# Kernel tuning notes

Measured on AMD Instinct MI355X. Metric: run time of the kernel, lower is better.

The kernel has to match this reference:

```python
import jax, jax.numpy as jnp
import numpy as np

SL, BS, D, H = 2048, 4, 512, 8
NH = D // H  # per-head dim (nhid)
SCALE = np.float32(1.0 / np.sqrt(NH))


def setup_inputs() -> dict:
    key = jax.random.key(0)
    ks = jax.random.split(key, 8)
    s = np.float32(0.02)
    return {
        "input_tensor": jax.random.normal(ks[0], (SL, BS, D), jnp.float32),
        "keys_vector": jax.random.normal(ks[1], (SL, BS, D), jnp.float32),
        "values_vector": jax.random.normal(ks[2], (SL, BS, D), jnp.float32),
        # learned projections: query/keys/values -> num_heads*nhid, plus output proj
        "Wq": jax.random.normal(ks[3], (D, D), jnp.float32) * s,
        "bq": jnp.zeros((D,), jnp.float32),
        "Wk": jax.random.normal(ks[4], (D, D), jnp.float32) * s,
        "bk": jnp.zeros((D,), jnp.float32),
        "Wv": jax.random.normal(ks[5], (D, D), jnp.float32) * s,
        "bv": jnp.zeros((D,), jnp.float32),
        "Wo": jax.random.normal(ks[6], (D, D), jnp.float32) * s,
        "bo": jnp.zeros((D,), jnp.float32),
    }


def reference(input_tensor, keys_vector, values_vector, Wq, bq, Wk, bk, Wv, bv, Wo, bo):
    # Vectorized equivalent of the per-step Python loop with incremental mask
    # (mask=True): query step i attends to keys 0..i -> causal attention.
    q = (input_tensor @ Wq + bq).reshape(SL, BS, H, NH)   # [q,b,h,n]
    k = (keys_vector @ Wk + bk).reshape(SL, BS, H, NH)    # [s,b,h,n]
    v = (values_vector @ Wv + bv).reshape(SL, BS, H, NH)  # [s,b,h,n]
    scores = jnp.einsum('qbhn,sbhn->qsbh', q, k) * SCALE  # [q,s,b,h]
    causal = jnp.tril(jnp.ones((SL, SL), dtype=bool))     # allow s <= q
    scores = jnp.where(causal[:, :, None, None], scores, jnp.float32(-1e9))
    w = jax.nn.softmax(scores, axis=1)                    # softmax over keys s
    out = jnp.einsum('qsbh,sbhn->qbhn', w, v).reshape(SL, BS, D)
    return out @ Wo + bo                                  # [q,b,D]
```

## Files before the change

### kernel.cpp

```cpp
#include <hip/hip_runtime.h>

typedef __attribute__((ext_vector_type(8))) short short8;
typedef __attribute__((ext_vector_type(4))) short short4v;
typedef __attribute__((ext_vector_type(4))) float f32x4;
typedef __attribute__((ext_vector_type(2))) unsigned int uint2v;

constexpr int SL = 2048, BS = 4, D = 512, H = 8, NH = 64;
constexpr int M_ROWS = SL * BS;
constexpr float SCALE = 0.125f;
constexpr float LOG2E = 1.44269504088896340736f;

__device__ __forceinline__ unsigned short f2bf(float f) {
  union { float f; unsigned u; } v; v.f = f;
  unsigned r = v.u + 0x7FFFu + ((v.u >> 16) & 1u);
  return (unsigned short)(r >> 16);
}

__device__ __forceinline__ unsigned cvt_pk_bf16(float a, float b) {
  unsigned r;
  asm("v_cvt_pk_bf16_f32 %0, %1, %2" : "=v"(r) : "v"(a), "v"(b));
  return r;
}

__device__ __forceinline__ float fast_exp2(float x) {
  float r;
  asm("v_exp_f32 %0, %1" : "=v"(r) : "v"(x));
  return r;
}

__device__ __forceinline__ void gl16(const void* g, void* l) {
  __builtin_amdgcn_global_load_lds(
      (const __attribute__((address_space(1))) unsigned int*)g,
      (__attribute__((address_space(3))) unsigned int*)l, 16, 0, 0);
}

__global__ __launch_bounds__(256) void prep_wt(
    const float* __restrict__ w0, const float* __restrict__ w1,
    const float* __restrict__ w2, const float* __restrict__ w3,
    unsigned short* __restrict__ wtb) {
  __shared__ float tl[64][65];
  const int tid = threadIdx.x;
  const int wi = blockIdx.x >> 6, t6 = blockIdx.x & 63;
  const int k0 = (t6 >> 3) * 64, n0 = (t6 & 7) * 64;
  const float* W = wi == 0 ? w0 : (wi == 1 ? w1 : (wi == 2 ? w2 : w3));
  unsigned short* WT = wtb + (size_t)wi * D * D;

#pragma unroll
  for (int i = 0; i < 4; ++i) {
    int k = (tid >> 4) + i * 16, n4 = (tid & 15) * 4;
    f32x4 v = *reinterpret_cast<const f32x4*>(&W[(size_t)(k0 + k) * D + n0 + n4]);
#pragma unroll
    for (int j = 0; j < 4; ++j) tl[n4 + j][k] = v[j];
  }
  __syncthreads();
#pragma unroll
  for (int i = 0; i < 2; ++i) {
    int n = (tid >> 3) + i * 32, k8 = (tid & 7) * 8;
    union { unsigned u[4]; short8 s; } pk;
#pragma unroll
    for (int j = 0; j < 4; ++j)
      pk.u[j] = cvt_pk_bf16(tl[n][k8 + 2 * j], tl[n][k8 + 2 * j + 1]);
    *reinterpret_cast<short8*>(&WT[(size_t)(n0 + n) * D + k0 + k8]) = pk.s;
  }
}

template <bool A_BF16, int OUT_MODE>
__device__ __forceinline__ void gemm_bt_body(const void* __restrict__ Ap,
                                             const unsigned short* __restrict__ BT,
                                             const float* __restrict__ bias,
                                             void* __restrict__ Outp, float scale,
                                             unsigned short* smem) {
  const int tid = threadIdx.x;
  const int brow = blockIdx.x * 128;
  const int bcol = blockIdx.y * 64;
  const int lane = tid & 63;
  const int wid = tid >> 6;
  const int wr = (wid >> 1) * 64;
  const int wc = (wid & 1) * 32;
  const int r = lane & 15;
  const int g = lane >> 4;

  auto a_buf = [&](int b) { return smem + b * 8192; };
  auto b_buf = [&](int b) { return smem + 16384 + b * 4096; };

  f32x4 acc[4][2];
#pragma unroll
  for (int m = 0; m < 4; ++m)
#pragma unroll
    for (int n = 0; n < 2; ++n) acc[m][n] = f32x4{0.f, 0.f, 0.f, 0.f};

  auto STAGE_B = [&](int kt, int bsel) {
    unsigned short* bl = b_buf(bsel);
#pragma unroll
    for (int j = 0; j < 2; ++j) {
      int c = j * 256 + tid;
      int row = c >> 3, c8 = (c & 7) ^ (row & 7);
      gl16(&BT[(size_t)(bcol + row) * D + kt + c8 * 8], &bl[c * 8]);
    }
  };
  auto STAGE_A_LDS = [&](int kt, int bsel) {
    const unsigned short* A = (const unsigned short*)Ap;
    unsigned short* al = a_buf(bsel);
#pragma unroll
    for (int j = 0; j < 4; ++j) {
      int c = j * 256 + tid;
      int row = c >> 3, c8 = (c & 7) ^ (row & 7);
      gl16(&A[(size_t)(brow + row) * D + kt + c8 * 8], &al[c * 8]);
    }
  };
  auto A_LOAD = [&](int kt, f32x4 (&va)[4][2]) {
    const float* A = (const float*)Ap;
#pragma unroll
    for (int j = 0; j < 4; ++j) {
      int c = j * 256 + tid;
      int row = c >> 3, c8 = (c & 7) ^ (row & 7);
      const float* ap = &A[(size_t)(brow + row) * D + kt + c8 * 8];
      va[j][0] = *reinterpret_cast<const f32x4*>(ap);
      va[j][1] = *reinterpret_cast<const f32x4*>(ap + 4);
    }
  };
  auto A_WRITE = [&](f32x4 (&va)[4][2], int bsel) {
    unsigned short* al = a_buf(bsel);
#pragma unroll
    for (int j = 0; j < 4; ++j) {
      int c = j * 256 + tid;
      union { unsigned u[4]; short8 s; } pk;
      pk.u[0] = cvt_pk_bf16(va[j][0][0], va[j][0][1]);
      pk.u[1] = cvt_pk_bf16(va[j][0][2], va[j][0][3]);
      pk.u[2] = cvt_pk_bf16(va[j][1][0], va[j][1][1]);
      pk.u[3] = cvt_pk_bf16(va[j][1][2], va[j][1][3]);
      *reinterpret_cast<short8*>(&al[c * 8]) = pk.s;
    }
  };
  auto COMPUTE = [&](int bsel) {
    const unsigned short* al = a_buf(bsel);
    const unsigned short* bl = b_buf(bsel);
#pragma unroll
    for (int kk2 = 0; kk2 < 2; ++kk2) {
      short8 af[4], bfr[2];
#pragma unroll
      for (int m = 0; m < 4; ++m)
        af[m] = *reinterpret_cast<const short8*>(
            &al[(wr + m * 16 + r) * 64 + (((kk2 * 4 + g) ^ (r & 7)) * 8)]);
#pragma unroll
      for (int n = 0; n < 2; ++n)
        bfr[n] = *reinterpret_cast<const short8*>(
            &bl[(wc + n * 16 + r) * 64 + (((kk2 * 4 + g) ^ (r & 7)) * 8)]);
      __builtin_amdgcn_s_setprio(1);
#pragma unroll
      for (int m = 0; m < 4; ++m)
#pragma unroll
        for (int n = 0; n < 2; ++n)
          acc[m][n] = __builtin_amdgcn_mfma_f32_16x16x32_bf16(af[m], bfr[n], acc[m][n], 0, 0, 0);
      __builtin_amdgcn_s_setprio(0);
    }
  };

  if (A_BF16) {
    STAGE_A_LDS(0, 0);
    STAGE_B(0, 0);
    asm volatile("s_waitcnt vmcnt(0)" ::: "memory");
  } else {
    f32x4 va[4][2];
    A_LOAD(0, va);
    STAGE_B(0, 0);
    asm volatile("s_waitcnt vmcnt(2)" ::: "memory");
    A_WRITE(va, 0);
    asm volatile("s_waitcnt vmcnt(0) lgkmcnt(0)" ::: "memory");
  }
  __builtin_amdgcn_s_barrier();

#pragma unroll
  for (int t = 0; t < 8; ++t) {
    const int cur = t & 1, nxt = cur ^ 1;
    const int ktn = (t + 1) * 64;
    __builtin_amdgcn_sched_barrier(0);
    f32x4 va[4][2];
    if (t < 7) {
      if (A_BF16) {
        STAGE_A_LDS(ktn, nxt);
        STAGE_B(ktn, nxt);
      } else {
        A_LOAD(ktn, va);
        STAGE_B(ktn, nxt);
      }
    }
    __builtin_amdgcn_sched_barrier(0);
    COMPUTE(cur);
    if (t < 7) {
      if (!A_BF16) {
        asm volatile("s_waitcnt vmcnt(2)" ::: "memory");
        A_WRITE(va, nxt);
      }
      asm volatile("s_waitcnt vmcnt(0) lgkmcnt(0)" ::: "memory");
      __builtin_amdgcn_s_barrier();
    }
  }

  if (OUT_MODE == 2) {
    __syncthreads();
    unsigned short* sc = smem;
    const int wr4 = wr >> 2;
#pragma unroll
    for (int m = 0; m < 4; ++m)
#pragma unroll
      for (int n = 0; n < 2; ++n) {
        int col = wc + n * 16 + r;
        float bv = bias[bcol + col];
        int sl = wr4 + m * 4 + g;
        int pp = ((sl >> 2) & 3) * 8 + ((sl >> 4) & 1) * 4 + (sl & 3);
#pragma unroll
        for (int rr = 0; rr < 4; ++rr) {
          int c = (rr * 4 + (pp >> 3)) ^ (col & 7);
          sc[col * 128 + c * 8 + (pp & 7)] = f2bf((acc[m][n][rr] + bv) * scale);
        }
      }
    asm volatile("s_waitcnt lgkmcnt(0)" ::: "memory");
    __builtin_amdgcn_s_barrier();
    unsigned short* VT = (unsigned short*)Outp;
    {
      int q = tid;
      int col = q >> 2, bb = q & 3;
      int gcol = bcol + col, hh = gcol >> 6, nh = gcol & 63;
      size_t gbase = (((size_t)bb * H + hh) * NH + nh) * SL + (brow >> 2);
#pragma unroll
      for (int j = 0; j < 4; ++j) {
        short8 v = *reinterpret_cast<const short8*>(
            &sc[col * 128 + (((bb * 4 + j) ^ (col & 7)) * 8)]);
        *reinterpret_cast<short8*>(&VT[gbase + j * 8]) = v;
      }
    }
  } else {
#pragma unroll
    for (int m = 0; m < 4; ++m)
#pragma unroll
      for (int n = 0; n < 2; ++n) {
        int gcol = bcol + wc + n * 16 + r;
        float bv = bias[gcol];
#pragma unroll
        for (int rr = 0; rr < 4; ++rr) {
          int grow = brow + wr + m * 16 + g * 4 + rr;
          float val = (acc[m][n][rr] + bv) * scale;
          if (OUT_MODE == 0)
            ((float*)Outp)[(size_t)grow * D + gcol] = val;
          else
            ((unsigned short*)Outp)[(size_t)grow * D + gcol] = f2bf(val);
        }
      }
  }
}

__global__ __launch_bounds__(256) void qkv_gemm(
    const float* __restrict__ x0, const float* __restrict__ x1, const float* __restrict__ x2,
    const unsigned short* __restrict__ wtb,
    const float* __restrict__ b0, const float* __restrict__ b1, const float* __restrict__ b2,
    unsigned short* __restrict__ q_out, unsigned short* __restrict__ k_out,
    unsigned short* __restrict__ vt_out) {
  __shared__ __align__(16) unsigned short smem[24576];
  int z = blockIdx.z;
  const float* X = z == 0 ? x0 : (z == 1 ? x1 : x2);
  const unsigned short* WT = wtb + (size_t)z * D * D;
  const float* B = z == 0 ? b0 : (z == 1 ? b1 : b2);
  float scale = (z == 0) ? SCALE * LOG2E : 1.0f;
  if (z == 2)
    gemm_bt_body<false, 2>(X, WT, B, vt_out, scale, smem);
  else
    gemm_bt_body<false, 1>(X, WT, B, z == 0 ? q_out : k_out, scale, smem);
}

__global__ __launch_bounds__(256) void gemm_oproj(
    const unsigned short* __restrict__ A, const unsigned short* __restrict__ WT,
    const float* __restrict__ B, float* __restrict__ Outp) {
  __shared__ __align__(16) unsigned short smem[24576];
  gemm_bt_body<true, 0>(A, WT, B, Outp, 1.0f, smem);
}

__global__ __launch_bounds__(256, 3) void flash_attn(
    const unsigned short* __restrict__ Q, const unsigned short* __restrict__ K,
    const unsigned short* __restrict__ Vt, unsigned short* __restrict__ O) {
  __shared__ __align__(16) unsigned short k_lds[3][64 * 64];
  __shared__ __align__(16) unsigned short v_lds[3][64 * 64];

  const int bid = blockIdx.x;
  const int s = bid >> 5, idx = bid & 31;
  const int grp = idx & 7;
  const int bh = grp * 4 + (idx >> 3);
  const int b = bh >> 3, h = bh & 7;
  const int qt = (s < 8) ? 31 - s : (s < 16) ? s + 8 : (s < 24) ? 31 - s : s - 24;
  const int q0 = qt * 64;

  const int tid = threadIdx.x;
  const int w = tid >> 6, lane = tid & 63;
  const int r = lane & 15, g = lane >> 4;
  const int swz = (r & 7) << 3;

  const unsigned short* Qb = Q + (size_t)b * D + h * NH;
  const unsigned short* Kb = K + (size_t)b * D + h * NH;
  const unsigned short* Vb = Vt + ((size_t)(b * H + h) * NH) * SL;
  unsigned short* Ob = O + (size_t)b * D + h * NH;

  auto STAGE = [&](int kt, int bsel) {
    unsigned short* kl = &k_lds[bsel][0];
    unsigned short* vl = &v_lds[bsel][0];
#pragma unroll
    for (int j = 0; j < 2; ++j) {
      int c = j * 256 + tid;
      int row = c >> 3, c8 = (c & 7) ^ (row & 7);
      gl16(&Kb[(size_t)(kt * 64 + row) * (BS * D) + c8 * 8], &kl[c * 8]);
      gl16(&Vb[(size_t)row * SL + kt * 64 + c8 * 8], &vl[c * 8]);
    }
  };

  STAGE(0, 0);
  if (qt >= 1) STAGE(1, 1);

  short8 qf[2];
#pragma unroll
  for (int kk = 0; kk < 2; ++kk)
    qf[kk] = *reinterpret_cast<const short8*>(
        &Qb[(size_t)(q0 + w * 16 + r) * (BS * D) + kk * 32 + g * 8]);

  f32x4 oa[4];
#pragma unroll
  for (int n = 0; n < 4; ++n) oa[n] = f32x4{0.f, 0.f, 0.f, 0.f};
  float mr = -1e30f, lrp = 0.f;

  int bsel = 0;
  for (int kt = 0; kt <= qt; ++kt) {
    if (kt < qt)
      asm volatile("s_waitcnt vmcnt(8)" ::: "memory");
    else
      asm volatile("s_waitcnt vmcnt(0)" ::: "memory");
    __builtin_amdgcn_s_barrier();
    __builtin_amdgcn_sched_barrier(0);
    if (kt + 2 <= qt) {
      int nb = bsel + 2; if (nb >= 3) nb -= 3;
      STAGE(kt + 2, nb);
    }

    const unsigned short* kl = &k_lds[bsel][0];
    const unsigned short* vl = &v_lds[bsel][0];
    short8 kf[2][4];
#pragma unroll
    for (int kk = 0; kk < 2; ++kk)
#pragma unroll
      for (int n = 0; n < 4; ++n)
        kf[kk][n] = *reinterpret_cast<const short8*>(
            &kl[(n * 16 + r) * 64 + ((kk * 32 + g * 8) ^ swz)]);

    f32x4 sv[4];
#pragma unroll
    for (int n = 0; n < 4; ++n) sv[n] = f32x4{0.f, 0.f, 0.f, 0.f};
#pragma unroll
    for (int kk = 0; kk < 2; ++kk)
#pragma unroll
      for (int n = 0; n < 4; ++n)
        sv[n] = __builtin_amdgcn_mfma_f32_16x16x32_bf16(kf[kk][n], qf[kk], sv[n], 0, 0, 0);

    short8 vt[2][4];
#pragma unroll
    for (int kk = 0; kk < 2; ++kk)
#pragma unroll
      for (int n = 0; n < 4; ++n)
        vt[kk][n] = *reinterpret_cast<const short8*>(
            &vl[(n * 16 + r) * 64 + ((kk * 32 + g * 8) ^ swz)]);

    if (kt == qt) {
      int qrow = q0 + w * 16 + r;
#pragma unroll
      for (int n = 0; n < 4; ++n)
#pragma unroll
        for (int rr = 0; rr < 4; ++rr)
          if (kt * 64 + n * 16 + g * 4 + rr > qrow) sv[n][rr] = -1e30f;
    }

    float t0 = fmaxf(fmaxf(sv[0][0], sv[0][1]), sv[0][2]);
    float t1 = fmaxf(fmaxf(sv[0][3], sv[1][0]), sv[1][1]);
    float t2 = fmaxf(fmaxf(sv[1][2], sv[1][3]), sv[2][0]);
    float t3 = fmaxf(fmaxf(sv[2][1], sv[2][2]), sv[2][3]);
    float t4 = fmaxf(fmaxf(sv[3][0], sv[3][1]), sv[3][2]);
    float mxl = fmaxf(fmaxf(fmaxf(t0, t1), fmaxf(t2, t3)), fmaxf(t4, sv[3][3]));
    bool need = __any(mxl > mr + 8.f);
    float mold = mr;
    float mnew = mold;
    if (need) {
      float mx = fmaxf(mxl, __shfl_xor(mxl, 16));
      mx = fmaxf(mx, __shfl_xor(mx, 32));
      mnew = fmaxf(mold, mx);
    }
#pragma unroll
    for (int n = 0; n < 4; ++n)
#pragma unroll
      for (int rr = 0; rr < 4; ++rr)
        sv[n][rr] = fast_exp2(sv[n][rr] - mnew);
    float a0 = (sv[0][0] + sv[0][1]) + (sv[0][2] + sv[0][3]);
    float a1 = (sv[1][0] + sv[1][1]) + (sv[1][2] + sv[1][3]);
    float a2 = (sv[2][0] + sv[2][1]) + (sv[2][2] + sv[2][3]);
    float a3 = (sv[3][0] + sv[3][1]) + (sv[3][2] + sv[3][3]);
    float psl = (a0 + a1) + (a2 + a3);
    if (need) {
      float sf = fast_exp2(mold - mnew);
      mr = mnew;
      lrp = lrp * sf + psl;
#pragma unroll
      for (int n = 0; n < 4; ++n) oa[n] *= sf;
    } else {
      lrp += psl;
    }

    short8 pf[2];
#pragma unroll
    for (int kk = 0; kk < 2; ++kk) {
      union { unsigned u[4]; short8 s8; } P;
      P.u[0] = cvt_pk_bf16(sv[2 * kk][0], sv[2 * kk][1]);
      P.u[1] = cvt_pk_bf16(sv[2 * kk][2], sv[2 * kk][3]);
      P.u[2] = cvt_pk_bf16(sv[2 * kk + 1][0], sv[2 * kk + 1][1]);
      P.u[3] = cvt_pk_bf16(sv[2 * kk + 1][2], sv[2 * kk + 1][3]);
      pf[kk] = P.s8;
    }

#pragma unroll
    for (int kk = 0; kk < 2; ++kk)
#pragma unroll
      for (int n = 0; n < 4; ++n)
        oa[n] = __builtin_amdgcn_mfma_f32_16x16x32_bf16(vt[kk][n], pf[kk], oa[n], 0, 0, 0);

    ++bsel; if (bsel >= 3) bsel = 0;
  }

  __syncthreads();
  {
    unsigned short* pw = &k_lds[0][0] + w * 2048;
    float lr = lrp + __shfl_xor(lrp, 16);
    lr += __shfl_xor(lr, 32);
    float inv = 1.0f / lr;
#pragma unroll
    for (int n = 0; n < 4; ++n) {
      uint2v pk;
      pk.x = cvt_pk_bf16(oa[n][0] * inv, oa[n][1] * inv);
      pk.y = cvt_pk_bf16(oa[n][2] * inv, oa[n][3] * inv);
      *reinterpret_cast<uint2v*>(&pw[r * 64 + ((n * 16 + g * 4) ^ swz)]) = pk;
    }
    asm volatile("s_waitcnt lgkmcnt(0)" ::: "memory");
    __builtin_amdgcn_sched_barrier(0);
#pragma unroll
    for (int i2 = 0; i2 < 2; ++i2) {
      int c = i2 * 64 + lane;
      int row = c >> 3, c8 = c & 7;
      short8 v = *reinterpret_cast<const short8*>(&pw[row * 64 + c8 * 8]);
      *reinterpret_cast<short8*>(
          &Ob[(size_t)(q0 + w * 16 + row) * (BS * D) + ((c8 ^ (row & 7)) * 8)]) = v;
    }
  }
}

extern "C" void kernel_launch(void* const* d_in, const int* in_sizes, int n_in,
                              void* d_out, int out_size, void* d_ws, size_t ws_size,
                              hipStream_t stream) {
  const float* x  = (const float*)d_in[0];
  const float* kx = (const float*)d_in[1];
  const float* vx = (const float*)d_in[2];
  const float* Wq = (const float*)d_in[3];
  const float* bq = (const float*)d_in[4];
  const float* Wk = (const float*)d_in[5];
  const float* bk = (const float*)d_in[6];
  const float* Wv = (const float*)d_in[7];
  const float* bv = (const float*)d_in[8];
  const float* Wo = (const float*)d_in[9];
  const float* bo = (const float*)d_in[10];

  unsigned short* ws = (unsigned short*)d_ws;
  unsigned short* qb  = ws;
  unsigned short* kb  = ws + (size_t)M_ROWS * D;
  unsigned short* vtb = ws + (size_t)M_ROWS * D * 2;
  unsigned short* wtb = ws + (size_t)M_ROWS * D * 3;

  prep_wt<<<dim3(256), dim3(256), 0, stream>>>(Wq, Wk, Wv, Wo, wtb);
  qkv_gemm<<<dim3(64, 8, 3), dim3(256), 0, stream>>>(x, kx, vx, wtb, bq, bk, bv,
                                                     qb, kb, vtb);
  flash_attn<<<dim3(1024), dim3(256), 0, stream>>>(qb, kb, vtb, qb);
  gemm_oproj<<<dim3(64, 8, 1), dim3(256), 0, stream>>>(qb, wtb + (size_t)3 * D * D,
                                                       bo, (float*)d_out);
}
```

Measured before the change: 80.30 us.

## Deepen GEMM k-loop pipeline to prefetch two tiles ahead with triple buffering

Restructures the shared GEMM body so global-to-LDS staging runs two k-tiles ahead instead of one. The oproj path uses three A and three B LDS buffers, and the QKV path keeps register-staged A double-buffered while B is triple-buffered. Partial vmcnt waits replace the full drains before each barrier, aiming to hide global load latency behind MFMA compute. This raises LDS usage per block, which may reduce occupancy, and relies on hand-tuned waitcnt values being correct.

After: 83.27 us. 1.04x slower.

```diff
diff --git a/kernel.cpp b/kernel.cpp
--- a/kernel.cpp
+++ b/kernel.cpp
@@ -80,8 +80,9 @@
   const int r = lane & 15;
   const int g = lane >> 4;
 
+  constexpr int A_BUFS = A_BF16 ? 3 : 2;
   auto a_buf = [&](int b) { return smem + b * 8192; };
-  auto b_buf = [&](int b) { return smem + 16384 + b * 4096; };
+  auto b_buf = [&](int b) { return smem + A_BUFS * 8192 + b * 4096; };
 
   f32x4 acc[4][2];
 #pragma unroll
@@ -132,8 +133,8 @@
       *reinterpret_cast<short8*>(&al[c * 8]) = pk.s;
     }
   };
-  auto COMPUTE = [&](int bsel) {
-    const unsigned short* al = a_buf(bsel);
+  auto COMPUTE = [&](int asel, int bsel) {
+    const unsigned short* al = a_buf(asel);
     const unsigned short* bl = b_buf(bsel);
 #pragma unroll
     for (int kk2 = 0; kk2 < 2; ++kk2) {
@@ -157,43 +158,49 @@
   };
 
   if (A_BF16) {
-    STAGE_A_LDS(0, 0);
-    STAGE_B(0, 0);
-    asm volatile("s_waitcnt vmcnt(0)" ::: "memory");
+    STAGE_A_LDS(0, 0);  STAGE_B(0, 0);
+    STAGE_A_LDS(64, 1); STAGE_B(64, 1);
+    asm volatile("s_waitcnt vmcnt(6)" ::: "memory");
+    __builtin_amdgcn_s_barrier();
+#pragma unroll
+    for (int t = 0; t < 8; ++t) {
+      __builtin_amdgcn_sched_barrier(0);
+      if (t < 6) { STAGE_A_LDS((t + 2) * 64, (t + 2) % 3); STAGE_B((t + 2) * 64, (t + 2) % 3); }
+      __builtin_amdgcn_sched_barrier(0);
+      COMPUTE(t % 3, t % 3);
+      if (t < 7) {
+        if (t < 6) asm volatile("s_waitcnt vmcnt(6)" ::: "memory");
+        else       asm volatile("s_waitcnt vmcnt(0)" ::: "memory");
+        __builtin_amdgcn_s_barrier();
+      }
+    }
   } else {
     f32x4 va[4][2];
     A_LOAD(0, va);
     STAGE_B(0, 0);
-    asm volatile("s_waitcnt vmcnt(2)" ::: "memory");
+    STAGE_B(64, 1);
+    asm volatile("s_waitcnt vmcnt(4)" ::: "memory");
     A_WRITE(va, 0);
-    asm volatile("s_waitcnt vmcnt(0) lgkmcnt(0)" ::: "memory");
-  }
-  __builtin_amdgcn_s_barrier();
-
-#pragma unroll
-  for (int t = 0; t < 8; ++t) {
-    const int cur = t & 1, nxt = cur ^ 1;
-    const int ktn = (t + 1) * 64;
-    __builtin_amdgcn_sched_barrier(0);
-    f32x4 va[4][2];
-    if (t < 7) {
-      if (A_BF16) {
-        STAGE_A_LDS(ktn, nxt);
-        STAGE_B(ktn, nxt);
-      } else {
-        A_LOAD(ktn, va);
-        STAGE_B(ktn, nxt);
-      }
-    }
-    __builtin_amdgcn_sched_barrier(0);
-    COMPUTE(cur);
-    if (t < 7) {
-      if (!A_BF16) {
-        asm volatile("s_waitcnt vmcnt(2)" ::: "memory");
-        A_WRITE(va, nxt);
-      }
-      asm volatile("s_waitcnt vmcnt(0) lgkmcnt(0)" ::: "memory");
-      __builtin_amdgcn_s_barrier();
+    A_LOAD(64, va);
+    asm volatile("s_waitcnt vmcnt(10)" ::: "memory");
+    asm volatile("s_waitcnt lgkmcnt(0)" ::: "memory");
+    __builtin_amdgcn_s_barrier();
+#pragma unroll
+    for (int t = 0; t < 8; ++t) {
+      __builtin_amdgcn_sched_barrier(0);
+      if (t < 6) STAGE_B((t + 2) * 64, (t + 2) % 3);
+      if (t < 7) {
+        if (t < 6) asm volatile("s_waitcnt vmcnt(2)" ::: "memory");
+        else       asm volatile("s_waitcnt vmcnt(0)" ::: "memory");
+        A_WRITE(va, (t + 1) & 1);
+        if (t < 6) A_LOAD((t + 2) * 64, va);
+      }
+      __builtin_amdgcn_sched_barrier(0);
+      COMPUTE(t & 1, t % 3);
+      if (t < 7) {
+        asm volatile("s_waitcnt lgkmcnt(0)" ::: "memory");
+        __builtin_amdgcn_s_barrier();
+      }
     }
   }
 
@@ -256,7 +263,7 @@
     const float* __restrict__ b0, const float* __restrict__ b1, const float* __restrict__ b2,
     unsigned short* __restrict__ q_out, unsigned short* __restrict__ k_out,
     unsigned short* __restrict__ vt_out) {
-  __shared__ __align__(16) unsigned short smem[24576];
+  __shared__ __align__(16) unsigned short smem[2 * 8192 + 3 * 4096];
   int z = blockIdx.z;
   const float* X = z == 0 ? x0 : (z == 1 ? x1 : x2);
   const unsigned short* WT = wtb + (size_t)z * D * D;
@@ -271,7 +278,7 @@
 __global__ __launch_bounds__(256) void gemm_oproj(
     const unsigned short* __restrict__ A, const unsigned short* __restrict__ WT,
     const float* __restrict__ B, float* __restrict__ Outp) {
-  __shared__ __align__(16) unsigned short smem[24576];
+  __shared__ __align__(16) unsigned short smem[3 * 8192 + 3 * 4096];
   gemm_bt_body<true, 0>(A, WT, B, Outp, 1.0f, smem);
 }
 
```

## Pre-convert activations to bf16 and use triple-buffered async-LDS GEMM

Applied to the files above, without the earlier changes.

Adds a standalone kernel that converts the three fp32 activation inputs to bf16 into scratch buffers (reusing d_out and the q/k workspaces with carefully ordered launches). The fused QKV GEMM is split into three bf16 GEMM launches that stage A via global_load_lds instead of register loads plus conversion. The GEMM pipeline moves from double to triple buffering with partial vmcnt waits so two k-tiles stay in flight. This costs an extra pass over the activations in memory and more kernel launches, and reduces grid parallelism per launch compared with the single z=3 launch.

Measured after the change: 91.95 us. 14.5% more time.

```diff
diff --git a/kernel.cpp b/kernel.cpp
--- a/kernel.cpp
+++ b/kernel.cpp
@@ -32,6 +32,27 @@
   __builtin_amdgcn_global_load_lds(
       (const __attribute__((address_space(1))) unsigned int*)g,
       (__attribute__((address_space(3))) unsigned int*)l, 16, 0, 0);
+}
+
+__global__ __launch_bounds__(256) void conv3(
+    const float* __restrict__ x0, const float* __restrict__ x1,
+    const float* __restrict__ x2,
+    unsigned short* __restrict__ d0, unsigned short* __restrict__ d1,
+    unsigned short* __restrict__ d2) {
+  const int u = blockIdx.x * 256 + threadIdx.x;
+#pragma unroll
+  for (int z = 0; z < 3; ++z) {
+    const float* src = z == 0 ? x0 : (z == 1 ? x1 : x2);
+    unsigned short* dst = z == 0 ? d0 : (z == 1 ? d1 : d2);
+    f32x4 v0 = *reinterpret_cast<const f32x4*>(&src[(size_t)u * 8]);
+    f32x4 v1 = *reinterpret_cast<const f32x4*>(&src[(size_t)u * 8 + 4]);
+    union { unsigned uu[4]; short8 s; } pk;
+    pk.uu[0] = cvt_pk_bf16(v0[0], v0[1]);
+    pk.uu[1] = cvt_pk_bf16(v0[2], v0[3]);
+    pk.uu[2] = cvt_pk_bf16(v1[0], v1[1]);
+    pk.uu[3] = cvt_pk_bf16(v1[2], v1[3]);
+    *reinterpret_cast<short8*>(&dst[(size_t)u * 8]) = pk.s;
+  }
 }
 
 __global__ __launch_bounds__(256) void prep_wt(
@@ -64,12 +85,12 @@
   }
 }
 
-template <bool A_BF16, int OUT_MODE>
-__device__ __forceinline__ void gemm_bt_body(const void* __restrict__ Ap,
-                                             const unsigned short* __restrict__ BT,
-                                             const float* __restrict__ bias,
-                                             void* __restrict__ Outp, float scale,
-                                             unsigned short* smem) {
+template <int OUT_MODE>
+__global__ __launch_bounds__(256) void gemm_bf16(
+    const unsigned short* __restrict__ Abf,
+    const unsigned short* __restrict__ BT,
+    const float* __restrict__ bias, void* __restrict__ Outp, float scale) {
+  __shared__ __align__(16) unsigned short smem[3 * 8192 + 3 * 4096];
   const int tid = threadIdx.x;
   const int brow = blockIdx.x * 128;
   const int bcol = blockIdx.y * 64;
@@ -81,7 +102,7 @@
   const int g = lane >> 4;
 
   auto a_buf = [&](int b) { return smem + b * 8192; };
-  auto b_buf = [&](int b) { return smem + 16384 + b * 4096; };
+  auto b_buf = [&](int b) { return smem + 3 * 8192 + b * 4096; };
 
   f32x4 acc[4][2];
 #pragma unroll
@@ -89,6 +110,15 @@
 #pragma unroll
     for (int n = 0; n < 2; ++n) acc[m][n] = f32x4{0.f, 0.f, 0.f, 0.f};
 
+  auto STAGE_A = [&](int kt, int bsel) {
+    unsigned short* al = a_buf(bsel);
+#pragma unroll
+    for (int j = 0; j < 4; ++j) {
+      int c = j * 256 + tid;
+      int row = c >> 3, c8 = (c & 7) ^ (row & 7);
+      gl16(&Abf[(size_t)(brow + row) * D + kt + c8 * 8], &al[c * 8]);
+    }
+  };
   auto STAGE_B = [&](int kt, int bsel) {
     unsigned short* bl = b_buf(bsel);
 #pragma unroll
@@ -98,40 +128,6 @@
       gl16(&BT[(size_t)(bcol + row) * D + kt + c8 * 8], &bl[c * 8]);
     }
   };
-  auto STAGE_A_LDS = [&](int kt, int bsel) {
-    const unsigned short* A = (const unsigned short*)Ap;
-    unsigned short* al = a_buf(bsel);
-#pragma unroll
-    for (int j = 0; j < 4; ++j) {
-      int c = j * 256 + tid;
-      int row = c >> 3, c8 = (c & 7) ^ (row & 7);
-      gl16(&A[(size_t)(brow + row) * D + kt + c8 * 8], &al[c * 8]);
-    }
-  };
-  auto A_LOAD = [&](int kt, f32x4 (&va)[4][2]) {
-    const float* A = (const float*)Ap;
-#pragma unroll
-    for (int j = 0; j < 4; ++j) {
-      int c = j * 256 + tid;
-      int row = c >> 3, c8 = (c & 7) ^ (row & 7);
-      const float* ap = &A[(size_t)(brow + row) * D + kt + c8 * 8];
-      va[j][0] = *reinterpret_cast<const f32x4*>(ap);
-      va[j][1] = *reinterpret_cast<const f32x4*>(ap + 4);
-    }
-  };
-  auto A_WRITE = [&](f32x4 (&va)[4][2], int bsel) {
-    unsigned short* al = a_buf(bsel);
-#pragma unroll
-    for (int j = 0; j < 4; ++j) {
-      int c = j * 256 + tid;
-      union { unsigned u[4]; short8 s; } pk;
-      pk.u[0] = cvt_pk_bf16(va[j][0][0], va[j][0][1]);
-      pk.u[1] = cvt_pk_bf16(va[j][0][2], va[j][0][3]);
-      pk.u[2] = cvt_pk_bf16(va[j][1][0], va[j][1][1]);
-      pk.u[3] = cvt_pk_bf16(va[j][1][2], va[j][1][3]);
-      *reinterpret_cast<short8*>(&al[c * 8]) = pk.s;
-    }
-  };
   auto COMPUTE = [&](int bsel) {
     const unsigned short* al = a_buf(bsel);
     const unsigned short* bl = b_buf(bsel);
@@ -156,43 +152,19 @@
     }
   };
 
-  if (A_BF16) {
-    STAGE_A_LDS(0, 0);
-    STAGE_B(0, 0);
-    asm volatile("s_waitcnt vmcnt(0)" ::: "memory");
-  } else {
-    f32x4 va[4][2];
-    A_LOAD(0, va);
-    STAGE_B(0, 0);
-    asm volatile("s_waitcnt vmcnt(2)" ::: "memory");
-    A_WRITE(va, 0);
-    asm volatile("s_waitcnt vmcnt(0) lgkmcnt(0)" ::: "memory");
-  }
+  STAGE_A(0, 0);  STAGE_B(0, 0);
+  STAGE_A(64, 1); STAGE_B(64, 1);
+  asm volatile("s_waitcnt vmcnt(6)" ::: "memory");
   __builtin_amdgcn_s_barrier();
-
 #pragma unroll
   for (int t = 0; t < 8; ++t) {
-    const int cur = t & 1, nxt = cur ^ 1;
-    const int ktn = (t + 1) * 64;
     __builtin_amdgcn_sched_barrier(0);
-    f32x4 va[4][2];
+    if (t < 6) { STAGE_A((t + 2) * 64, (t + 2) % 3); STAGE_B((t + 2) * 64, (t + 2) % 3); }
+    __builtin_amdgcn_sched_barrier(0);
+    COMPUTE(t % 3);
     if (t < 7) {
-      if (A_BF16) {
-        STAGE_A_LDS(ktn, nxt);
-        STAGE_B(ktn, nxt);
-      } else {
-        A_LOAD(ktn, va);
-        STAGE_B(ktn, nxt);
-      }
-    }
-    __builtin_amdgcn_sched_barrier(0);
-    COMPUTE(cur);
-    if (t < 7) {
-      if (!A_BF16) {
-        asm volatile("s_waitcnt vmcnt(2)" ::: "memory");
-        A_WRITE(va, nxt);
-      }
-      asm volatile("s_waitcnt vmcnt(0) lgkmcnt(0)" ::: "memory");
+      if (t < 6) asm volatile("s_waitcnt vmcnt(6)" ::: "memory");
+      else       asm volatile("s_waitcnt vmcnt(0)" ::: "memory");
       __builtin_amdgcn_s_barrier();
     }
   }
@@ -248,31 +220,6 @@
         }
       }
   }
-}
-
-__global__ __launch_bounds__(256) void qkv_gemm(
-    const float* __restrict__ x0, const float* __restrict__ x1, const float* __restrict__ x2,
-    const unsigned short* __restrict__ wtb,
-    const float* __restrict__ b0, const float* __restrict__ b1, const float* __restrict__ b2,
-    unsigned short* __restrict__ q_out, unsigned short* __restrict__ k_out,
-    unsigned short* __restrict__ vt_out) {
-  __shared__ __align__(16) unsigned short smem[24576];
-  int z = blockIdx.z;
-  const float* X = z == 0 ? x0 : (z == 1 ? x1 : x2);
-  const unsigned short* WT = wtb + (size_t)z * D * D;
-  const float* B = z == 0 ? b0 : (z == 1 ? b1 : b2);
-  float scale = (z == 0) ? SCALE * LOG2E : 1.0f;
-  if (z == 2)
-    gemm_bt_body<false, 2>(X, WT, B, vt_out, scale, smem);
-  else
-    gemm_bt_body<false, 1>(X, WT, B, z == 0 ? q_out : k_out, scale, smem);
-}
-
-__global__ __launch_bounds__(256) void gemm_oproj(
-    const unsigned short* __restrict__ A, const unsigned short* __restrict__ WT,
-    const float* __restrict__ B, float* __restrict__ Outp) {
-  __shared__ __align__(16) unsigned short smem[24576];
-  gemm_bt_body<true, 0>(A, WT, B, Outp, 1.0f, smem);
 }
 
 __global__ __launch_bounds__(256, 3) void flash_attn(
@@ -474,11 +421,13 @@
   unsigned short* kb  = ws + (size_t)M_ROWS * D;
   unsigned short* vtb = ws + (size_t)M_ROWS * D * 2;
   unsigned short* wtb = ws + (size_t)M_ROWS * D * 3;
+  unsigned short* xscratch = (unsigned short*)d_out;
 
   prep_wt<<<dim3(256), dim3(256), 0, stream>>>(Wq, Wk, Wv, Wo, wtb);
-  qkv_gemm<<<dim3(64, 8, 3), dim3(256), 0, stream>>>(x, kx, vx, wtb, bq, bk, bv,
-                                                     qb, kb, vtb);
+  conv3<<<dim3(2048), dim3(256), 0, stream>>>(x, kx, vx, xscratch, qb, kb);
+  gemm_bf16<2><<<dim3(64, 8), dim3(256), 0, stream>>>(kb, wtb + (size_t)2 * D * D, bv, vtb, 1.0f);
+  gemm_bf16<1><<<dim3(64, 8), dim3(256), 0, stream>>>(qb, wtb + (size_t)1 * D * D, bk, kb, 1.0f);
+  gemm_bf16<1><<<dim3(64, 8), dim3(256), 0, stream>>>(xscratch, wtb, bq, qb, SCALE * LOG2E);
   flash_attn<<<dim3(1024), dim3(256), 0, stream>>>(qb, kb, vtb, qb);
-  gemm_oproj<<<dim3(64, 8, 1), dim3(256), 0, stream>>>(qb, wtb + (size_t)3 * D * D,
-                                                       bo, (float*)d_out);
-}
+  gemm_bf16<0><<<dim3(64, 8), dim3(256), 0, stream>>>(qb, wtb + (size_t)3 * D * D, bo, d_out, 1.0f);
+}
```
